# Kernel optimization log

Measured on AMD Instinct MI355X. Metric: run time of the kernel, lower is better.

The kernel has to match this reference:

```python
import jax, jax.numpy as jnp
import numpy as np

NUM_HEADS = 12
EMBED_DIM = 768
QUERY_DIM = 384
HEAD_DIM = EMBED_DIM // NUM_HEADS


def setup_inputs() -> dict:
    key = jax.random.key(0)
    ks = jax.random.split(key, 10)
    R, L, B = 64, 512, 4
    x = jax.random.normal(ks[0], (R, L, B, EMBED_DIM), dtype=jnp.float32)
    query = jax.random.normal(ks[1], (L, B, QUERY_DIM), dtype=jnp.float32)
    s = 0.02
    Wq = jax.random.normal(ks[2], (EMBED_DIM, QUERY_DIM), dtype=jnp.float32) * s
    bq = jnp.zeros((EMBED_DIM,), dtype=jnp.float32)
    Wk = jax.random.normal(ks[3], (EMBED_DIM, EMBED_DIM), dtype=jnp.float32) * s
    bk = jnp.zeros((EMBED_DIM,), dtype=jnp.float32)
    Wv = jax.random.normal(ks[4], (EMBED_DIM, EMBED_DIM), dtype=jnp.float32) * s
    bv = jnp.zeros((EMBED_DIM,), dtype=jnp.float32)
    Wo = jax.random.normal(ks[5], (EMBED_DIM, EMBED_DIM), dtype=jnp.float32) * s
    bo = jnp.zeros((EMBED_DIM,), dtype=jnp.float32)
    return {"x": x, "query": query, "Wq": Wq, "bq": bq, "Wk": Wk, "bk": bk,
            "Wv": Wv, "bv": bv, "Wo": Wo, "bo": bo}


def reference(x, query, Wq, bq, Wk, bk, Wv, bv, Wo, bo):
    R, L, B, E = x.shape
    H, D = NUM_HEADS, HEAD_DIM
    # scaling = head_dim^-0.5 / sqrt(num_rows)
    scaling = (D ** -0.5) / np.sqrt(R)
    # q: [L, B, H, D]
    q = (query @ Wq.T + bq).reshape(L, B, H, D)
    # k: [R, L, B, H, D], pre-scaled
    k = ((x @ Wk.T + bk) * scaling).reshape(R, L, B, H, D)
    # row-summed attention logits: sum over r and d -> [H, B, i, j]
    attn_weights = jnp.einsum('jnhd,rinhd->hnij', q, k)
    attn_probs = jax.nn.softmax(attn_weights, axis=-1)
    # v: [R, L, B, H, D]
    v = (x @ Wv.T + bv).reshape(R, L, B, H, D)
    # context: [R, i, B, H, D] -> [R, L, B, E]
    context = jnp.einsum('hnij,rjnhd->rinhd', attn_probs, v).reshape(R, L, B, E)
    output = context @ Wo.T + bo
    return (output, attn_probs)
```

## Files before the change

### kernel.cpp

```cpp
#include <hip/hip_runtime.h>
#include <stdint.h>


#define R_ 64
#define L_ 512
#define B_ 4
#define E_ 768
#define H_ 12
#define D_ 64
#define P_ (L_*B_*E_)
#define MBIG_ (R_*L_*B_)
#define OUT0_ 100663296

typedef unsigned short u16;
typedef short short8 __attribute__((ext_vector_type(8)));
typedef float float4v __attribute__((ext_vector_type(4)));

__device__ __forceinline__ u16 f2bf(float f) {
  union { float f; uint32_t u; } v; v.f = f;
  return (u16)((v.u + 0x7fffu + ((v.u >> 16) & 1u)) >> 16);
}

__device__ __forceinline__ void gload16(const u16* g, u16* lds) {
  __builtin_amdgcn_global_load_lds(
      (const __attribute__((address_space(1))) u16*)g,
      (__attribute__((address_space(3))) u16*)lds, 16, 0, 0);
}

#define SWZB(d) ((((d) ^ ((d) >> 3)) & 7) << 3)

__global__ __launch_bounds__(256) void k_wconv(const float* __restrict__ Wv,
                                               const float* __restrict__ Wo,
                                               u16* __restrict__ Wvb,
                                               u16* __restrict__ Wob) {
  int i4 = (blockIdx.x * 256 + threadIdx.x) * 4;
  float4 v = *(const float4*)(Wv + i4);
  ushort4 b; b.x = f2bf(v.x); b.y = f2bf(v.y); b.z = f2bf(v.z); b.w = f2bf(v.w);
  *(ushort4*)(Wvb + i4) = b;
  float4 o = *(const float4*)(Wo + i4);
  ushort4 c; c.x = f2bf(o.x); c.y = f2bf(o.y); c.z = f2bf(o.z); c.w = f2bf(o.w);
  *(ushort4*)(Wob + i4) = c;
}

__global__ __launch_bounds__(256) void k_xprep(const float* __restrict__ x,
                                               u16* __restrict__ xbf,
                                               float* __restrict__ xsum) {
  size_t p4 = ((size_t)blockIdx.x * 256 + threadIdx.x) * 4;
  float sx = 0.f, sy = 0.f, sz = 0.f, sw = 0.f;
  for (int r = 0; r < R_; ++r) {
    float4 v = *(const float4*)(x + (size_t)r * P_ + p4);
    sx += v.x; sy += v.y; sz += v.z; sw += v.w;
    ushort4 b; b.x = f2bf(v.x); b.y = f2bf(v.y); b.z = f2bf(v.z); b.w = f2bf(v.w);
    *(ushort4*)(xbf + (size_t)r * P_ + p4) = b;
  }
  float4 s; s.x = sx; s.y = sy; s.z = sz; s.w = sw;
  *(float4*)(xsum + p4) = s;
}

__global__ __launch_bounds__(256) void k_gemm_f32(const float* __restrict__ A,
                                                  const float* __restrict__ W,
                                                  const float* __restrict__ bias,
                                                  float* __restrict__ C,
                                                  int M, int N, int K, float alpha) {
  __shared__ float sA[16][65], sW[16][65];
  const int t = threadIdx.x;
  const int col0 = blockIdx.x * 64, row0 = blockIdx.y * 64;
  const int tx = t & 15, ty = t >> 4;
  const int srow = t >> 2, sk4 = (t & 3) * 4;
  float acc[4][4] = {};
  for (int kt = 0; kt < K; kt += 16) {
    float4 va = *(const float4*)&A[(size_t)(row0 + srow) * K + kt + sk4];
    sA[sk4 + 0][srow] = va.x; sA[sk4 + 1][srow] = va.y;
    sA[sk4 + 2][srow] = va.z; sA[sk4 + 3][srow] = va.w;
    float4 vw = *(const float4*)&W[(size_t)(col0 + srow) * K + kt + sk4];
    sW[sk4 + 0][srow] = vw.x; sW[sk4 + 1][srow] = vw.y;
    sW[sk4 + 2][srow] = vw.z; sW[sk4 + 3][srow] = vw.w;
    __syncthreads();
#pragma unroll
    for (int k = 0; k < 16; ++k) {
      float ar[4], wr[4];
#pragma unroll
      for (int a = 0; a < 4; ++a) ar[a] = sA[k][ty + 16 * a];
#pragma unroll
      for (int b = 0; b < 4; ++b) wr[b] = sW[k][tx + 16 * b];
#pragma unroll
      for (int a = 0; a < 4; ++a)
#pragma unroll
        for (int b = 0; b < 4; ++b) acc[a][b] += ar[a] * wr[b];
    }
    __syncthreads();
  }
#pragma unroll
  for (int a = 0; a < 4; ++a)
#pragma unroll
    for (int b = 0; b < 4; ++b) {
      int col = col0 + tx + 16 * b;
      C[(size_t)(row0 + ty + 16 * a) * N + col] = alpha * acc[a][b] + bias[col];
    }
}

__global__ __launch_bounds__(256) void k_logits_softmax(const float* __restrict__ q,
                                                        const float* __restrict__ ksum,
                                                        float* __restrict__ probsF,
                                                        u16* __restrict__ probsB) {
  __shared__ float sk[16][65];
  __shared__ float sq[64][65];
  const int t = threadIdx.x;
  const int it = blockIdx.x;
  const int hn = blockIdx.y;
  const int h = hn >> 2, n = hn & 3;
  const int ii = t >> 4, jx = t & 15;
  {
    const float* src = ksum + ((size_t)(it * 16 + ii) * 4 + n) * 768 + h * 64 + jx * 4;
    float4 v = *(const float4*)src;
    sk[ii][jx * 4 + 0] = v.x; sk[ii][jx * 4 + 1] = v.y;
    sk[ii][jx * 4 + 2] = v.z; sk[ii][jx * 4 + 3] = v.w;
  }
  float lg[32];
  for (int jt = 0; jt < 8; ++jt) {
#pragma unroll
    for (int p = 0; p < 4; ++p) {
      int c = p * 256 + t;
      int row = c >> 4, c4 = (c & 15) * 4;
      const float* src = q + ((size_t)(jt * 64 + row) * 4 + n) * 768 + h * 64 + c4;
      float4 v = *(const float4*)src;
      sq[row][c4 + 0] = v.x; sq[row][c4 + 1] = v.y;
      sq[row][c4 + 2] = v.z; sq[row][c4 + 3] = v.w;
    }
    __syncthreads();
    float s0 = 0.f, s1 = 0.f, s2 = 0.f, s3 = 0.f;
#pragma unroll
    for (int d = 0; d < 64; ++d) {
      float a = sk[ii][d];
      s0 += a * sq[jx][d];
      s1 += a * sq[jx + 16][d];
      s2 += a * sq[jx + 32][d];
      s3 += a * sq[jx + 48][d];
    }
    lg[jt * 4 + 0] = s0; lg[jt * 4 + 1] = s1; lg[jt * 4 + 2] = s2; lg[jt * 4 + 3] = s3;
    __syncthreads();
  }
  float mx = -1e30f;
#pragma unroll
  for (int u = 0; u < 32; ++u) mx = fmaxf(mx, lg[u]);
  for (int off = 1; off <= 8; off <<= 1) mx = fmaxf(mx, __shfl_xor(mx, off, 64));
  float sm = 0.f;
#pragma unroll
  for (int u = 0; u < 32; ++u) { lg[u] = expf(lg[u] - mx); sm += lg[u]; }
  for (int off = 1; off <= 8; off <<= 1) sm += __shfl_xor(sm, off, 64);
  float inv = 1.0f / sm;
  size_t rowbase = ((size_t)hn * 512 + it * 16 + ii) * 512;
#pragma unroll
  for (int jt = 0; jt < 8; ++jt)
#pragma unroll
    for (int qq = 0; qq < 4; ++qq) {
      int j = jt * 64 + qq * 16 + jx;
      float val = lg[jt * 4 + qq] * inv;
      probsF[rowbase + j] = val;
      probsB[rowbase + j] = f2bf(val);
    }
}

__global__ __launch_bounds__(256) void k_gemm_v(const u16* __restrict__ A,
                                                const u16* __restrict__ W,
                                                const float* __restrict__ bias,
                                                u16* __restrict__ V) {
  __shared__ __align__(16) u16 lA[128 * 64];
  __shared__ __align__(16) u16 lB[128 * 64];
  const int t = threadIdx.x;
  const int wave = t >> 6, lane = t & 63;
  const int row0 = blockIdx.x * 128, col0 = blockIdx.y * 128;
  const int wr = (wave >> 1) * 64, wc = (wave & 1) * 64;
  const int l16 = lane & 15, l4 = lane >> 4;
  float4v acc[4][4] = {};
  for (int kt = 0; kt < 768; kt += 64) {
#pragma unroll
    for (int p = 0; p < 4; ++p) {
      int c = p * 256 + t;
      int row = c >> 3, k8 = (c & 7) * 8;
      gload16(&A[(size_t)(row0 + row) * 768 + kt + k8], &lA[(size_t)c * 8]);
      gload16(&W[(size_t)(col0 + row) * 768 + kt + k8], &lB[(size_t)c * 8]);
    }
    __syncthreads();
#pragma unroll
    for (int kc = 0; kc < 64; kc += 32) {
      short8 af[4], bf[4];
#pragma unroll
      for (int i = 0; i < 4; ++i) af[i] = *(short8*)&lA[(wr + i * 16 + l16) * 64 + kc + l4 * 8];
#pragma unroll
      for (int j = 0; j < 4; ++j) bf[j] = *(short8*)&lB[(wc + j * 16 + l16) * 64 + kc + l4 * 8];
#pragma unroll
      for (int i = 0; i < 4; ++i)
#pragma unroll
        for (int j = 0; j < 4; ++j)
          acc[i][j] = __builtin_amdgcn_mfma_f32_16x16x32_bf16(af[i], bf[j], acc[i][j], 0, 0, 0);
    }
    __syncthreads();
  }
#pragma unroll
  for (int i = 0; i < 4; ++i)
#pragma unroll
    for (int j = 0; j < 4; ++j) {
      int e = col0 + wc + j * 16 + l16;
      float bi = bias[e];
#pragma unroll
      for (int rg = 0; rg < 4; ++rg) {
        int m = row0 + wr + i * 16 + l4 * 4 + rg;
        V[(size_t)m * 768 + e] = f2bf(acc[i][j][rg] + bi);
      }
    }
}

__global__ __launch_bounds__(256) void k_gemm_ctx(const u16* __restrict__ P,
                                                  const u16* __restrict__ V,
                                                  u16* __restrict__ CTX) {
  __shared__ __align__(16) u16 lA[256 * 64];
  __shared__ __align__(16) u16 lB[64 * 64];
  const int t = threadIdx.x;
  const int wave = t >> 6, lane = t & 63;
  const int half = blockIdx.x;
  const int slice = blockIdx.y;
  const int h = slice % 12, rn = slice / 12, n = rn & 3, r = rn >> 2;
  const u16* Ps = P + ((size_t)(h * 4 + n)) * 512 * 512 + (size_t)half * 256 * 512;
  const u16* Vs = V + ((size_t)r * 2048 + n) * 768 + h * 64;
  const int wi = wave * 64;
  const int l16 = lane & 15, l4 = lane >> 4;
  float4v acc[4][4] = {};
  for (int jt = 0; jt < 512; jt += 64) {
#pragma unroll
    for (int p = 0; p < 8; ++p) {
      int c = p * 256 + t;
      int row = c >> 3, k8 = (c & 7) * 8;
      gload16(&Ps[(size_t)row * 512 + jt + k8], &lA[(size_t)c * 8]);
    }
#pragma unroll
    for (int p = 0; p < 2; ++p) {
      int c = p * 256 + t;
      int j = c >> 3, d8 = (c & 7) * 8;
      short8 v = *(const short8*)&Vs[(size_t)(jt + j) * 3072 + d8];
#pragma unroll
      for (int u = 0; u < 8; ++u) {
        int d = d8 + u;
        lB[d * 64 + (j ^ SWZB(d))] = (u16)v[u];
      }
    }
    __syncthreads();
#pragma unroll
    for (int kc = 0; kc < 64; kc += 32) {
      short8 af[4], bf[4];
#pragma unroll
      for (int i = 0; i < 4; ++i) af[i] = *(short8*)&lA[(wi + i * 16 + l16) * 64 + kc + l4 * 8];
#pragma unroll
      for (int j = 0; j < 4; ++j) {
        int d = j * 16 + l16;
        bf[j] = *(short8*)&lB[d * 64 + ((kc + l4 * 8) ^ SWZB(d))];
      }
#pragma unroll
      for (int i = 0; i < 4; ++i)
#pragma unroll
        for (int j = 0; j < 4; ++j)
          acc[i][j] = __builtin_amdgcn_mfma_f32_16x16x32_bf16(af[i], bf[j], acc[i][j], 0, 0, 0);
    }
    __syncthreads();
  }
#pragma unroll
  for (int i = 0; i < 4; ++i)
#pragma unroll
    for (int j = 0; j < 4; ++j) {
      int d = j * 16 + l16;
#pragma unroll
      for (int rg = 0; rg < 4; ++rg) {
        int ii = half * 256 + wi + i * 16 + l4 * 4 + rg;
        size_t m = ((size_t)(r * 512 + ii)) * 4 + n;
        CTX[m * 768 + h * 64 + d] = f2bf(acc[i][j][rg]);
      }
    }
}

__global__ __launch_bounds__(256) void k_gemm_out(const u16* __restrict__ A,
                                                  const u16* __restrict__ W,
                                                  const float* __restrict__ bias,
                                                  float* __restrict__ OUT) {
  __shared__ __align__(16) u16 lA[128 * 64];
  __shared__ __align__(16) u16 lB[128 * 64];
  const int t = threadIdx.x;
  const int wave = t >> 6, lane = t & 63;
  const int row0 = blockIdx.x * 128, col0 = blockIdx.y * 128;
  const int wr = (wave >> 1) * 64, wc = (wave & 1) * 64;
  const int l16 = lane & 15, l4 = lane >> 4;
  float4v acc[4][4] = {};
  for (int kt = 0; kt < 768; kt += 64) {
#pragma unroll
    for (int p = 0; p < 4; ++p) {
      int c = p * 256 + t;
      int row = c >> 3, k8 = (c & 7) * 8;
      gload16(&A[(size_t)(row0 + row) * 768 + kt + k8], &lA[(size_t)c * 8]);
      gload16(&W[(size_t)(col0 + row) * 768 + kt + k8], &lB[(size_t)c * 8]);
    }
    __syncthreads();
#pragma unroll
    for (int kc = 0; kc < 64; kc += 32) {
      short8 af[4], bf[4];
#pragma unroll
      for (int i = 0; i < 4; ++i) af[i] = *(short8*)&lA[(wr + i * 16 + l16) * 64 + kc + l4 * 8];
#pragma unroll
      for (int j = 0; j < 4; ++j) bf[j] = *(short8*)&lB[(wc + j * 16 + l16) * 64 + kc + l4 * 8];
#pragma unroll
      for (int i = 0; i < 4; ++i)
#pragma unroll
        for (int j = 0; j < 4; ++j)
          acc[i][j] = __builtin_amdgcn_mfma_f32_16x16x32_bf16(af[i], bf[j], acc[i][j], 0, 0, 0);
    }
    __syncthreads();
  }
#pragma unroll
  for (int i = 0; i < 4; ++i)
#pragma unroll
    for (int j = 0; j < 4; ++j) {
      int e = col0 + wc + j * 16 + l16;
      float bi = bias[e];
#pragma unroll
      for (int rg = 0; rg < 4; ++rg) {
        int m = row0 + wr + i * 16 + l4 * 4 + rg;
        OUT[(size_t)m * 768 + e] = acc[i][j][rg] + bi;
      }
    }
}

static const size_t WS_CTX  = 0;
static const size_t WS_XSUM = 201326592;
static const size_t WS_Q    = WS_XSUM + 6291456;
static const size_t WS_KSUM = WS_Q + 6291456;
static const size_t WS_PBF  = WS_KSUM + 6291456;
static const size_t WS_WVB  = WS_PBF + 25165824;
static const size_t WS_WOB  = WS_WVB + 1179648;

extern "C" void kernel_launch(void* const* d_in, const int* in_sizes, int n_in,
                              void* d_out, int out_size, void* d_ws, size_t ws_size,
                              hipStream_t stream) {
  const float* x     = (const float*)d_in[0];
  const float* query = (const float*)d_in[1];
  const float* Wq    = (const float*)d_in[2];
  const float* bq    = (const float*)d_in[3];
  const float* Wk    = (const float*)d_in[4];
  const float* bk    = (const float*)d_in[5];
  const float* Wv    = (const float*)d_in[6];
  const float* bv    = (const float*)d_in[7];
  const float* Wo    = (const float*)d_in[8];
  const float* bo    = (const float*)d_in[9];
  char* ws = (char*)d_ws;
  u16*   xbf   = (u16*)(ws + WS_CTX);
  u16*   ctxb  = xbf;
  float* xsum  = (float*)(ws + WS_XSUM);
  float* qws   = (float*)(ws + WS_Q);
  float* ksum  = (float*)(ws + WS_KSUM);
  u16*   pbf   = (u16*)(ws + WS_PBF);
  u16*   wvb   = (u16*)(ws + WS_WVB);
  u16*   wob   = (u16*)(ws + WS_WOB);
  float* out0   = (float*)d_out;
  float* probsF = out0 + OUT0_;
  u16*   vnat   = (u16*)d_out;

  k_wconv<<<576, 256, 0, stream>>>(Wv, Wo, wvb, wob);
  k_xprep<<<1536, 256, 0, stream>>>(x, xbf, xsum);
  k_gemm_f32<<<dim3(12, 32), 256, 0, stream>>>(query, Wq, bq, qws, 2048, 768, 384, 1.0f);
  k_gemm_f32<<<dim3(12, 32), 256, 0, stream>>>(xsum, Wk, bk, ksum, 2048, 768, 768, 1.0f / 64.0f);
  k_logits_softmax<<<dim3(32, 48), 256, 0, stream>>>(qws, ksum, probsF, pbf);
  k_gemm_v<<<dim3(1024, 6), 256, 0, stream>>>(xbf, wvb, bv, vnat);
  k_gemm_ctx<<<dim3(2, 3072), 256, 0, stream>>>(pbf, vnat, ctxb);
  k_gemm_out<<<dim3(1024, 6), 256, 0, stream>>>(ctxb, wob, bo, out0);
}
```

Before: 1.701 ms.

## Emit V transposed per head from V GEMM and remap block order

The V projection now stages its output tile in LDS and writes V in a transposed [r,n,h,d,j] layout. This lets the context GEMM load V with direct global-to-LDS async loads instead of per-element transposing scalar LDS stores. All three large GEMMs now use a 1D grid with an XCD-aware block remapping, which groups blocks that share operands on the same chiplet for better L2 reuse. The cost is an extra LDS pass and more scattered writes in the V GEMM epilogue, plus a dependence on the remap matching the hardware's block dispatch.

Result: faster. 1.602 ms (-5.9%).

```diff
diff --git a/kernel.cpp b/kernel.cpp
--- a/kernel.cpp
+++ b/kernel.cpp
@@ -26,8 +26,6 @@
       (const __attribute__((address_space(1))) u16*)g,
       (__attribute__((address_space(3))) u16*)lds, 16, 0, 0);
 }
-
-#define SWZB(d) ((((d) ^ ((d) >> 3)) & 7) << 3)
 
 __global__ __launch_bounds__(256) void k_wconv(const float* __restrict__ Wv,
                                                const float* __restrict__ Wo,
@@ -161,15 +159,20 @@
     }
 }
 
+#define ECS(mr, ec) ((ec) ^ (((mr) & 7) << 3))
+
 __global__ __launch_bounds__(256) void k_gemm_v(const u16* __restrict__ A,
                                                 const u16* __restrict__ W,
                                                 const float* __restrict__ bias,
-                                                u16* __restrict__ V) {
-  __shared__ __align__(16) u16 lA[128 * 64];
-  __shared__ __align__(16) u16 lB[128 * 64];
+                                                u16* __restrict__ VT) {
+  __shared__ __align__(16) u16 smem[128 * 128];
+  u16* lA = smem;
+  u16* lB = smem + 128 * 64;
   const int t = threadIdx.x;
   const int wave = t >> 6, lane = t & 63;
-  const int row0 = blockIdx.x * 128, col0 = blockIdx.y * 128;
+  const int w = (blockIdx.x & 7) * 768 + (blockIdx.x >> 3);
+  const int ct = w % 6, rt = w / 6;
+  const int row0 = rt * 128, col0 = ct * 128;
   const int wr = (wave >> 1) * 64, wc = (wave & 1) * 64;
   const int l16 = lane & 15, l4 = lane >> 4;
   float4v acc[4][4] = {};
@@ -201,28 +204,51 @@
   for (int i = 0; i < 4; ++i)
 #pragma unroll
     for (int j = 0; j < 4; ++j) {
-      int e = col0 + wc + j * 16 + l16;
-      float bi = bias[e];
+      int ec = wc + j * 16 + l16;
+      float bi = bias[col0 + ec];
 #pragma unroll
       for (int rg = 0; rg < 4; ++rg) {
-        int m = row0 + wr + i * 16 + l4 * 4 + rg;
-        V[(size_t)m * 768 + e] = f2bf(acc[i][j][rg] + bi);
+        int mr = wr + i * 16 + l4 * 4 + rg;
+        smem[mr * 128 + ECS(mr, ec)] = f2bf(acc[i][j][rg] + bi);
       }
     }
+  __syncthreads();
+  const int r = row0 >> 11;
+  const int j0 = (row0 >> 2) & 511;
+  const int h0 = col0 >> 6;
+#pragma unroll
+  for (int up = 0; up < 2; ++up) {
+    int u = up * 256 + t;
+    int n = u & 3, d = (u >> 2) & 63, hh = u >> 8;
+    u16* dst = VT + (((size_t)(r * 4 + n) * 12 + (h0 + hh)) * 64 + d) * 512 + j0;
+    int ec = hh * 64 + d;
+#pragma unroll
+    for (int g = 0; g < 4; ++g) {
+      short8 v;
+#pragma unroll
+      for (int e8 = 0; e8 < 8; ++e8) {
+        int mr = (g * 8 + e8) * 4 + n;
+        v[e8] = (short)smem[mr * 128 + ECS(mr, ec)];
+      }
+      *(short8*)(dst + g * 8) = v;
+    }
+  }
 }
 
 __global__ __launch_bounds__(256) void k_gemm_ctx(const u16* __restrict__ P,
-                                                  const u16* __restrict__ V,
+                                                  const u16* __restrict__ VT,
                                                   u16* __restrict__ CTX) {
   __shared__ __align__(16) u16 lA[256 * 64];
   __shared__ __align__(16) u16 lB[64 * 64];
   const int t = threadIdx.x;
   const int wave = t >> 6, lane = t & 63;
-  const int half = blockIdx.x;
-  const int slice = blockIdx.y;
-  const int h = slice % 12, rn = slice / 12, n = rn & 3, r = rn >> 2;
-  const u16* Ps = P + ((size_t)(h * 4 + n)) * 512 * 512 + (size_t)half * 256 * 512;
-  const u16* Vs = V + ((size_t)r * 2048 + n) * 768 + h * 64;
+  const int w = (blockIdx.x & 7) * 768 + (blockIdx.x >> 3);
+  const int half = w & 1;
+  const int y = w >> 1;
+  const int r = y & 63, q = y >> 6;
+  const int n = q & 3, h = q >> 2;
+  const u16* Ps = P + ((size_t)q) * 512 * 512 + (size_t)half * 256 * 512;
+  const u16* Vs = VT + ((size_t)(r * 4 + n) * 12 + h) * 64 * 512;
   const int wi = wave * 64;
   const int l16 = lane & 15, l4 = lane >> 4;
   float4v acc[4][4] = {};
@@ -236,13 +262,8 @@
 #pragma unroll
     for (int p = 0; p < 2; ++p) {
       int c = p * 256 + t;
-      int j = c >> 3, d8 = (c & 7) * 8;
-      short8 v = *(const short8*)&Vs[(size_t)(jt + j) * 3072 + d8];
-#pragma unroll
-      for (int u = 0; u < 8; ++u) {
-        int d = d8 + u;
-        lB[d * 64 + (j ^ SWZB(d))] = (u16)v[u];
-      }
+      int row = c >> 3, k8 = (c & 7) * 8;
+      gload16(&Vs[(size_t)row * 512 + jt + k8], &lB[(size_t)c * 8]);
     }
     __syncthreads();
 #pragma unroll
@@ -251,10 +272,7 @@
 #pragma unroll
       for (int i = 0; i < 4; ++i) af[i] = *(short8*)&lA[(wi + i * 16 + l16) * 64 + kc + l4 * 8];
 #pragma unroll
-      for (int j = 0; j < 4; ++j) {
-        int d = j * 16 + l16;
-        bf[j] = *(short8*)&lB[d * 64 + ((kc + l4 * 8) ^ SWZB(d))];
-      }
+      for (int j = 0; j < 4; ++j) bf[j] = *(short8*)&lB[(j * 16 + l16) * 64 + kc + l4 * 8];
 #pragma unroll
       for (int i = 0; i < 4; ++i)
 #pragma unroll
@@ -285,7 +303,9 @@
   __shared__ __align__(16) u16 lB[128 * 64];
   const int t = threadIdx.x;
   const int wave = t >> 6, lane = t & 63;
-  const int row0 = blockIdx.x * 128, col0 = blockIdx.y * 128;
+  const int w = (blockIdx.x & 7) * 768 + (blockIdx.x >> 3);
+  const int ct = w % 6, rt = w / 6;
+  const int row0 = rt * 128, col0 = ct * 128;
   const int wr = (wave >> 1) * 64, wc = (wave & 1) * 64;
   const int l16 = lane & 15, l4 = lane >> 4;
   float4v acc[4][4] = {};
@@ -359,14 +379,14 @@
   u16*   wob   = (u16*)(ws + WS_WOB);
   float* out0   = (float*)d_out;
   float* probsF = out0 + OUT0_;
-  u16*   vnat   = (u16*)d_out;
+  u16*   vt     = (u16*)d_out;
 
   k_wconv<<<576, 256, 0, stream>>>(Wv, Wo, wvb, wob);
   k_xprep<<<1536, 256, 0, stream>>>(x, xbf, xsum);
   k_gemm_f32<<<dim3(12, 32), 256, 0, stream>>>(query, Wq, bq, qws, 2048, 768, 384, 1.0f);
   k_gemm_f32<<<dim3(12, 32), 256, 0, stream>>>(xsum, Wk, bk, ksum, 2048, 768, 768, 1.0f / 64.0f);
   k_logits_softmax<<<dim3(32, 48), 256, 0, stream>>>(qws, ksum, probsF, pbf);
-  k_gemm_v<<<dim3(1024, 6), 256, 0, stream>>>(xbf, wvb, bv, vnat);
-  k_gemm_ctx<<<dim3(2, 3072), 256, 0, stream>>>(pbf, vnat, ctxb);
-  k_gemm_out<<<dim3(1024, 6), 256, 0, stream>>>(ctxb, wob, bo, out0);
-}
+  k_gemm_v<<<6144, 256, 0, stream>>>(xbf, wvb, bv, vt);
+  k_gemm_ctx<<<6144, 256, 0, stream>>>(pbf, vt, ctxb);
+  k_gemm_out<<<6144, 256, 0, stream>>>(ctxb, wob, bo, out0);
+}
```
